# Performance work log

Hardware: AMD Instinct MI355X
Metric: run time of the kernel (lower is better)

## Reference

```python
import jax, jax.numpy as jnp
import numpy as np

B, C, N = 32, 128, 64
HID = 2 * C
STEEPNESS = 50.0


def _bitonic_layers(n):
    """Index pairs (a, b) for each compare-exchange layer of a bitonic sorting
    network, matching diffsort's bitonic_network construction."""
    num_blocks = int(np.log2(n))
    assert n == 2 ** num_blocks
    layers = []
    for block in range(num_blocks):
        for layer in range(block + 1):
            m = 2 ** (block - layer)
            a_idx, b_idx = [], []
            for i in range(0, n, 2 * m):
                for j in range(m):
                    ix = i + j
                    a, b = ix, ix + m
                    # alternate direction within bitonic blocks
                    if (ix // 2 ** (block + 1)) % 2 == 1:
                        a, b = b, a
                    a_idx.append(a)
                    b_idx.append(b)
            layers.append((np.asarray(a_idx), np.asarray(b_idx)))
    return layers

_LAYERS = _bitonic_layers(N)  # 21 layers for N=64


def _diff_sort(scores):
    """Differentiable bitonic sort (diffsort, distribution='cauchy').
    Returns (soft-sorted scores, soft permutation matrix P) with
    sorted = scores @ P; the module applies P via bmm(P, rows)."""
    b, n = scores.shape
    x = scores
    P = jnp.broadcast_to(jnp.eye(n, dtype=scores.dtype), (b, n, n))
    inv_pi = 1.0 / np.pi
    for a_idx, b_idx in _LAYERS:
        xa, xb = x[:, a_idx], x[:, b_idx]
        alpha = jnp.arctan((xb - xa) * STEEPNESS) * inv_pi + 0.5  # Cauchy CDF
        x = x.at[:, a_idx].set(alpha * xa + (1.0 - alpha) * xb)
        x = x.at[:, b_idx].set((1.0 - alpha) * xa + alpha * xb)
        Pa, Pb = P[:, :, a_idx], P[:, :, b_idx]
        al = alpha[:, None, :]
        P = P.at[:, :, a_idx].set(al * Pa + (1.0 - al) * Pb)
        P = P.at[:, :, b_idx].set((1.0 - al) * Pa + al * Pb)
    return x, P


def setup_inputs() -> dict:
    key = jax.random.key(0)
    ks = jax.random.split(key, 9)
    s = 0.05  # keep score magnitudes reasonable under steepness=50
    return {
        "x": jax.random.normal(ks[0], (B, C, N, N), jnp.float32),
        "w1": jax.random.normal(ks[1], (HID, C), jnp.float32) * s,
        "b1": jax.random.normal(ks[2], (HID,), jnp.float32) * s,
        "w2": jax.random.normal(ks[3], (HID, HID), jnp.float32) * s,
        "b2": jax.random.normal(ks[4], (HID,), jnp.float32) * s,
        "w_row": jax.random.normal(ks[5], (HID, N), jnp.float32) * s,
        "b_row": jax.random.normal(ks[6], (1,), jnp.float32) * s,
        "w_col": jax.random.normal(ks[7], (HID, N), jnp.float32) * s,
        "b_col": jax.random.normal(ks[8], (1,), jnp.float32) * s,
    }


def reference(x, w1, b1, w2, b2, w_row, b_row, w_col, b_col):
    # feat_extractor: two 1x1 convs (pointwise channel GEMMs) + ReLU
    h = jax.nn.relu(jnp.einsum('bchw,oc->bohw', x, w1) + b1[None, :, None, None])
    h = jax.nn.relu(jnp.einsum('bchw,oc->bohw', h, w2) + b2[None, :, None, None])

    # row branch: Conv1d(HID*N,1,1) over flattened (channel, width) per row
    row_scores = jnp.einsum('bchw,cw->bh', h, w_row) + b_row  # (B, N)
    _, p_row = _diff_sort(row_scores)
    x = jnp.einsum('bij,bcjk->bcik', p_row, x)  # bmm(P_row, x) per channel

    # col branch: Conv1d(HID*N,1,1) over flattened (channel, height) per column
    col_scores = jnp.einsum('bchw,ch->bw', h, w_col) + b_col  # (B, N)
    _, p_col = _diff_sort(col_scores)
    # original: bmm(P_col, x^T) then view as (B,C,N,N) with NO transpose back
    x = jnp.einsum('bij,bckj->bcik', p_col, x)
    return x
```

## Files before the change

### kernel.cpp

```cpp
#include <hip/hip_runtime.h>
#include <math.h>

#define B_    32
#define C_    128
#define N_    64
#define HID_  256
#define PIX_  4096
#define STEEP 50.0f
#define INV_PI 0.318309886183790671f
#define LDA   40
#define LDH   272
#define LDX   72

typedef unsigned short u16;
typedef __attribute__((ext_vector_type(8))) short bf16x8;
typedef __attribute__((ext_vector_type(4))) float f32x4;

__device__ __forceinline__ u16 f2bf(float f) {
    unsigned int u = __builtin_bit_cast(unsigned int, f);
    unsigned int r = (u + 0x7FFFu + ((u >> 16) & 1u)) >> 16;
    return (u16)r;
}
__device__ __forceinline__ float bf2f(u16 h) {
    unsigned int u = ((unsigned int)h) << 16;
    return __builtin_bit_cast(float, u);
}

__global__ void k0_init(float* __restrict__ col_s, const float* __restrict__ b_col) {
    int i = blockIdx.x * 256 + threadIdx.x;
    if (i < B_ * N_) col_s[i] = b_col[0];
}

__global__ void k_prep(const float* __restrict__ w1, const float* __restrict__ w2,
                       u16* __restrict__ w1h, u16* __restrict__ w1l,
                       u16* __restrict__ w2h, u16* __restrict__ w2l) {
    int i = blockIdx.x * 256 + threadIdx.x;
    if (i < HID_ * C_) {
        float v = w1[i];
        u16 h = f2bf(v);
        w1h[i] = h;
        w1l[i] = f2bf(v - bf2f(h));
    } else {
        int j = i - HID_ * C_;
        if (j < HID_ * HID_) {
            float v = w2[j];
            u16 h = f2bf(v);
            w2h[j] = h;
            w2l[j] = f2bf(v - bf2f(h));
        }
    }
}

__global__ __launch_bounds__(256) void k12_fused(
    const float* __restrict__ x,
    const u16* __restrict__ w1h, const u16* __restrict__ w1l,
    const float* __restrict__ b1,
    const u16* __restrict__ w2h, const u16* __restrict__ w2l,
    const float* __restrict__ b2, const float* __restrict__ w_row,
    const float* __restrict__ b_row, const float* __restrict__ w_col,
    float* __restrict__ row_s, float* __restrict__ col_s) {
    __shared__ __align__(16) u16 Lh1h[64 * LDH];
    __shared__ __align__(16) u16 Lh1l[64 * LDH];
    __shared__ __align__(16) u16 Bh[64 * LDA];
    __shared__ __align__(16) u16 Bl[64 * LDA];
    __shared__ float col_red[64];
    __shared__ float row_red;

    const int t = threadIdx.x;
    const int l = t & 63, w = t >> 6;
    const int col = l & 15, q = l >> 4;
    const int hrow = blockIdx.x;
    const int b = blockIdx.y;
    const int pbase = hrow * 64;
    const float* xb = x + (size_t)b * C_ * PIX_ + pbase;

    if (t < 64) col_red[t] = 0.f;
    if (t == 0) row_red = 0.f;

    f32x4 acc[4][4];
#pragma unroll
    for (int i = 0; i < 4; i++)
#pragma unroll
        for (int j = 0; j < 4; j++) acc[i][j] = (f32x4){0.f, 0.f, 0.f, 0.f};

    const int pt = t & 15, ct = t >> 4;
    for (int kc = 0; kc < 4; kc++) {
        const int c0 = kc * 32;
        {
            const float* r0 = &xb[(size_t)(c0 + 2 * ct) * PIX_ + pt * 4];
            const float* r1 = &xb[(size_t)(c0 + 2 * ct + 1) * PIX_ + pt * 4];
            float4 v0 = *(const float4*)r0;
            float4 v1 = *(const float4*)r1;
            float a0[4] = {v0.x, v0.y, v0.z, v0.w};
            float a1[4] = {v1.x, v1.y, v1.z, v1.w};
#pragma unroll
            for (int j = 0; j < 4; j++) {
                u16 h0 = f2bf(a0[j]), h1 = f2bf(a1[j]);
                u16 l0 = f2bf(a0[j] - bf2f(h0)), l1 = f2bf(a1[j] - bf2f(h1));
                *(unsigned int*)&Bh[(pt * 4 + j) * LDA + 2 * ct] =
                    (unsigned int)h0 | ((unsigned int)h1 << 16);
                *(unsigned int*)&Bl[(pt * 4 + j) * LDA + 2 * ct] =
                    (unsigned int)l0 | ((unsigned int)l1 << 16);
            }
        }
        __syncthreads();
        bf16x8 ah[4], al_[4], bh[4], bl[4];
#pragma unroll
        for (int mf = 0; mf < 4; mf++) {
            size_t ro = (size_t)(64 * w + 16 * mf + col) * C_ + c0 + q * 8;
            ah[mf] = *(const bf16x8*)&w1h[ro];
            al_[mf] = *(const bf16x8*)&w1l[ro];
        }
#pragma unroll
        for (int nt = 0; nt < 4; nt++) {
            bh[nt] = *(const bf16x8*)&Bh[(nt * 16 + col) * LDA + q * 8];
            bl[nt] = *(const bf16x8*)&Bl[(nt * 16 + col) * LDA + q * 8];
        }
#pragma unroll
        for (int mf = 0; mf < 4; mf++)
#pragma unroll
            for (int nt = 0; nt < 4; nt++) {
                acc[mf][nt] = __builtin_amdgcn_mfma_f32_16x16x32_bf16(ah[mf], bh[nt], acc[mf][nt], 0, 0, 0);
                acc[mf][nt] = __builtin_amdgcn_mfma_f32_16x16x32_bf16(ah[mf], bl[nt], acc[mf][nt], 0, 0, 0);
                acc[mf][nt] = __builtin_amdgcn_mfma_f32_16x16x32_bf16(al_[mf], bh[nt], acc[mf][nt], 0, 0, 0);
            }
        __syncthreads();
    }

#pragma unroll
    for (int mf = 0; mf < 4; mf++) {
        int o = 64 * w + 16 * mf + q * 4;
        float bias[4];
#pragma unroll
        for (int r = 0; r < 4; r++) bias[r] = b1[o + r];
#pragma unroll
        for (int nt = 0; nt < 4; nt++) {
            int p = nt * 16 + col;
            u16 hh[4], ll[4];
#pragma unroll
            for (int r = 0; r < 4; r++) {
                float v = fmaxf(acc[mf][nt][r] + bias[r], 0.f);
                u16 h = f2bf(v);
                hh[r] = h;
                ll[r] = f2bf(v - bf2f(h));
            }
            *(unsigned long long*)&Lh1h[p * LDH + o] =
                (unsigned long long)hh[0] | ((unsigned long long)hh[1] << 16) |
                ((unsigned long long)hh[2] << 32) | ((unsigned long long)hh[3] << 48);
            *(unsigned long long*)&Lh1l[p * LDH + o] =
                (unsigned long long)ll[0] | ((unsigned long long)ll[1] << 16) |
                ((unsigned long long)ll[2] << 32) | ((unsigned long long)ll[3] << 48);
        }
    }
    __syncthreads();

    f32x4 acc2[4][4];
#pragma unroll
    for (int i = 0; i < 4; i++)
#pragma unroll
        for (int j = 0; j < 4; j++) acc2[i][j] = (f32x4){0.f, 0.f, 0.f, 0.f};

    for (int kc = 0; kc < 8; kc++) {
        const int k0 = kc * 32;
        bf16x8 ah[4], al_[4], bh[4], bl[4];
#pragma unroll
        for (int mf = 0; mf < 4; mf++) {
            size_t ro = (size_t)(64 * w + 16 * mf + col) * HID_ + k0 + q * 8;
            ah[mf] = *(const bf16x8*)&w2h[ro];
            al_[mf] = *(const bf16x8*)&w2l[ro];
        }
#pragma unroll
        for (int nt = 0; nt < 4; nt++) {
            bh[nt] = *(const bf16x8*)&Lh1h[(nt * 16 + col) * LDH + k0 + q * 8];
            bl[nt] = *(const bf16x8*)&Lh1l[(nt * 16 + col) * LDH + k0 + q * 8];
        }
#pragma unroll
        for (int mf = 0; mf < 4; mf++)
#pragma unroll
            for (int nt = 0; nt < 4; nt++) {
                acc2[mf][nt] = __builtin_amdgcn_mfma_f32_16x16x32_bf16(ah[mf], bh[nt], acc2[mf][nt], 0, 0, 0);
                acc2[mf][nt] = __builtin_amdgcn_mfma_f32_16x16x32_bf16(ah[mf], bl[nt], acc2[mf][nt], 0, 0, 0);
                acc2[mf][nt] = __builtin_amdgcn_mfma_f32_16x16x32_bf16(al_[mf], bh[nt], acc2[mf][nt], 0, 0, 0);
            }
    }

    float rpart = 0.f;
    float cpart[4] = {0.f, 0.f, 0.f, 0.f};
#pragma unroll
    for (int mf = 0; mf < 4; mf++) {
        int o = 64 * w + 16 * mf + q * 4;
#pragma unroll
        for (int r = 0; r < 4; r++) {
            float bias = b2[o + r];
            float wcv = w_col[(o + r) * N_ + hrow];
#pragma unroll
            for (int nt = 0; nt < 4; nt++) {
                int wc = nt * 16 + col;
                float v = fmaxf(acc2[mf][nt][r] + bias, 0.f);
                rpart += v * w_row[(o + r) * N_ + wc];
                cpart[nt] += v * wcv;
            }
        }
    }
#pragma unroll
    for (int off = 32; off; off >>= 1) rpart += __shfl_xor(rpart, off, 64);
    if (l == 0) atomicAdd(&row_red, rpart);
#pragma unroll
    for (int nt = 0; nt < 4; nt++) {
        float cp = cpart[nt];
        cp += __shfl_xor(cp, 16, 64);
        cp += __shfl_xor(cp, 32, 64);
        if (l < 16) atomicAdd(&col_red[nt * 16 + l], cp);
    }
    __syncthreads();
    if (t < 64) atomicAdd(&col_s[b * N_ + t], col_red[t]);
    if (t == 0) row_s[b * N_ + hrow] = b_row[0] + row_red;
}

__global__ __launch_bounds__(256) void k4_diffsort(const float* __restrict__ row_s,
                                                   const float* __restrict__ col_s,
                                                   u16* __restrict__ prow_h, u16* __restrict__ prow_l,
                                                   u16* __restrict__ pcol_h, u16* __restrict__ pcol_l) {
    __shared__ float Ps[64 * 65];
    __shared__ float xs[64];
    __shared__ float als[32];
    const int t = threadIdx.x;
    const int which = blockIdx.x & 1;
    const int b = blockIdx.x >> 1;
    const float* sc = which ? col_s : row_s;
    u16* Ph = which ? pcol_h : prow_h;
    u16* Pl = which ? pcol_l : prow_l;

    if (t < 64) xs[t] = sc[b * 64 + t];
#pragma unroll
    for (int k = 0; k < 16; k++) {
        int idx = t + k * 256;
        int i = idx >> 6, j = idx & 63;
        Ps[i * 65 + j] = (i == j) ? 1.f : 0.f;
    }
    __syncthreads();

    const int r = t & 63, pg = t >> 6;
    for (int bl = 0; bl < 6; bl++) {
        for (int ly = 0; ly <= bl; ly++) {
            int sh = bl - ly;
            int m = 1 << sh;
            if (t < 32) {
                int i = (t >> sh) << (sh + 1);
                int j = t & (m - 1);
                int ix = i + j;
                int a = ix, bi = ix + m;
                if ((ix >> (bl + 1)) & 1) { int tmp = a; a = bi; bi = tmp; }
                float xa = xs[a], xbv = xs[bi];
                float al = atanf((xbv - xa) * STEEP) * INV_PI + 0.5f;
                als[t] = al;
                xs[a] = al * xa + (1.f - al) * xbv;
                xs[bi] = (1.f - al) * xa + al * xbv;
            }
            __syncthreads();
#pragma unroll
            for (int pi = 0; pi < 8; pi++) {
                int p = pg * 8 + pi;
                int i = (p >> sh) << (sh + 1);
                int j = p & (m - 1);
                int ix = i + j;
                int a = ix, bi = ix + m;
                if ((ix >> (bl + 1)) & 1) { int tmp = a; a = bi; bi = tmp; }
                float al = als[p];
                float Pa = Ps[r * 65 + a], Pb = Ps[r * 65 + bi];
                Ps[r * 65 + a] = al * Pa + (1.f - al) * Pb;
                Ps[r * 65 + bi] = (1.f - al) * Pa + al * Pb;
            }
            __syncthreads();
        }
    }
#pragma unroll
    for (int k = 0; k < 16; k++) {
        int idx = t + k * 256;
        int i = idx >> 6, j = idx & 63;
        float v = Ps[i * 65 + j];
        u16 h = f2bf(v);
        Ph[b * 4096 + idx] = h;
        Pl[b * 4096 + idx] = f2bf(v - bf2f(h));
    }
}

__global__ __launch_bounds__(256) void k5_permute(const float* __restrict__ x,
                                                  const u16* __restrict__ pcol_h,
                                                  const u16* __restrict__ pcol_l,
                                                  const u16* __restrict__ prow_h,
                                                  const u16* __restrict__ prow_l,
                                                  float* __restrict__ out) {
    __shared__ __align__(16) u16 Xh[64 * LDX];
    __shared__ __align__(16) u16 Xl[64 * LDX];
    __shared__ __align__(16) u16 Zh[64 * LDX];
    __shared__ __align__(16) u16 Zl[64 * LDX];
    const int t = threadIdx.x;
    const int l = t & 63, w = t >> 6;
    const int col = l & 15, q = l >> 4;
    const int b = blockIdx.y;
    const int cbase = blockIdx.x * 4;
    const int i0 = w * 16;

    const u16* pch = pcol_h + (size_t)b * 4096;
    const u16* pcl = pcol_l + (size_t)b * 4096;
    const u16* prh = prow_h + (size_t)b * 4096;
    const u16* prl = prow_l + (size_t)b * 4096;

    bf16x8 pcA_h[2], pcA_l[2];
#pragma unroll
    for (int ks = 0; ks < 2; ks++) {
        pcA_h[ks] = *(const bf16x8*)&pch[(i0 + col) * 64 + q * 8 + ks * 32];
        pcA_l[ks] = *(const bf16x8*)&pcl[(i0 + col) * 64 + q * 8 + ks * 32];
    }

    for (int ci = 0; ci < 4; ci++) {
        const int c = cbase + ci;
        const float* xc = x + ((size_t)b * C_ + c) * PIX_;
#pragma unroll
        for (int k = 0; k < 4; k++) {
            int f = t + k * 256;
            int rw = f >> 4, c4 = f & 15;
            float4 v = *(const float4*)&xc[f * 4];
            u16 h0 = f2bf(v.x), h1 = f2bf(v.y), h2 = f2bf(v.z), h3 = f2bf(v.w);
            ushort4 hv = {h0, h1, h2, h3};
            ushort4 lv = {f2bf(v.x - bf2f(h0)), f2bf(v.y - bf2f(h1)),
                          f2bf(v.z - bf2f(h2)), f2bf(v.w - bf2f(h3))};
            *(ushort4*)&Xh[rw * LDX + c4 * 4] = hv;
            *(ushort4*)&Xl[rw * LDX + c4 * 4] = lv;
        }
        __syncthreads();

        f32x4 acc[4];
#pragma unroll
        for (int nt = 0; nt < 4; nt++) acc[nt] = (f32x4){0.f, 0.f, 0.f, 0.f};
#pragma unroll
        for (int ks = 0; ks < 2; ks++) {
            bf16x8 ah = pcA_h[ks], al_ = pcA_l[ks];
#pragma unroll
            for (int nt = 0; nt < 4; nt++) {
                bf16x8 bh = *(const bf16x8*)&Xh[(nt * 16 + col) * LDX + q * 8 + ks * 32];
                bf16x8 bl = *(const bf16x8*)&Xl[(nt * 16 + col) * LDX + q * 8 + ks * 32];
                acc[nt] = __builtin_amdgcn_mfma_f32_16x16x32_bf16(ah, bh, acc[nt], 0, 0, 0);
                acc[nt] = __builtin_amdgcn_mfma_f32_16x16x32_bf16(ah, bl, acc[nt], 0, 0, 0);
                acc[nt] = __builtin_amdgcn_mfma_f32_16x16x32_bf16(al_, bh, acc[nt], 0, 0, 0);
            }
        }
#pragma unroll
        for (int nt = 0; nt < 4; nt++)
#pragma unroll
            for (int r = 0; r < 4; r++) {
                float v = acc[nt][r];
                u16 h = f2bf(v);
                int rw = i0 + q * 4 + r;
                Zh[rw * LDX + nt * 16 + col] = h;
                Zl[rw * LDX + nt * 16 + col] = f2bf(v - bf2f(h));
            }

        f32x4 acc2[4];
#pragma unroll
        for (int nt = 0; nt < 4; nt++) acc2[nt] = (f32x4){0.f, 0.f, 0.f, 0.f};
#pragma unroll
        for (int ks = 0; ks < 2; ks++) {
            bf16x8 ah = *(const bf16x8*)&Zh[(i0 + col) * LDX + q * 8 + ks * 32];
            bf16x8 al_ = *(const bf16x8*)&Zl[(i0 + col) * LDX + q * 8 + ks * 32];
#pragma unroll
            for (int nt = 0; nt < 4; nt++) {
                bf16x8 bh = *(const bf16x8*)&prh[(nt * 16 + col) * 64 + q * 8 + ks * 32];
                bf16x8 bl = *(const bf16x8*)&prl[(nt * 16 + col) * 64 + q * 8 + ks * 32];
                acc2[nt] = __builtin_amdgcn_mfma_f32_16x16x32_bf16(ah, bh, acc2[nt], 0, 0, 0);
                acc2[nt] = __builtin_amdgcn_mfma_f32_16x16x32_bf16(ah, bl, acc2[nt], 0, 0, 0);
                acc2[nt] = __builtin_amdgcn_mfma_f32_16x16x32_bf16(al_, bh, acc2[nt], 0, 0, 0);
            }
        }
        float* oc = out + ((size_t)b * C_ + c) * PIX_;
#pragma unroll
        for (int nt = 0; nt < 4; nt++)
#pragma unroll
            for (int r = 0; r < 4; r++)
                oc[(i0 + q * 4 + r) * 64 + nt * 16 + col] = acc2[nt][r];
        __syncthreads();
    }
}

extern "C" void kernel_launch(void* const* d_in, const int* in_sizes, int n_in,
                              void* d_out, int out_size, void* d_ws, size_t ws_size,
                              hipStream_t stream) {
    const float* x = (const float*)d_in[0];
    const float* w1 = (const float*)d_in[1];
    const float* b1 = (const float*)d_in[2];
    const float* w2 = (const float*)d_in[3];
    const float* b2 = (const float*)d_in[4];
    const float* w_row = (const float*)d_in[5];
    const float* b_row = (const float*)d_in[6];
    const float* w_col = (const float*)d_in[7];
    const float* b_col = (const float*)d_in[8];
    float* out = (float*)d_out;

    char* ws = (char*)d_ws;
    u16* w1h = (u16*)(ws);
    u16* w1l = (u16*)(ws + 65536);
    u16* w2h = (u16*)(ws + 131072);
    u16* w2l = (u16*)(ws + 262144);
    float* row_s = (float*)(ws + 393216);
    float* col_s = (float*)(ws + 401408);
    u16* prow_h = (u16*)(ws + 409600);
    u16* prow_l = (u16*)(ws + 671744);
    u16* pcol_h = (u16*)(ws + 933888);
    u16* pcol_l = (u16*)(ws + 1196032);

    hipLaunchKernelGGL(k0_init, dim3(8), dim3(256), 0, stream, col_s, b_col);
    hipLaunchKernelGGL(k_prep, dim3(384), dim3(256), 0, stream, w1, w2, w1h, w1l, w2h, w2l);
    hipLaunchKernelGGL(k12_fused, dim3(64, 32), dim3(256), 0, stream,
                       x, w1h, w1l, b1, w2h, w2l, b2, w_row, b_row, w_col, row_s, col_s);
    hipLaunchKernelGGL(k4_diffsort, dim3(64), dim3(256), 0, stream,
                       row_s, col_s, prow_h, prow_l, pcol_h, pcol_l);
    hipLaunchKernelGGL(k5_permute, dim3(32, 32), dim3(256), 0, stream,
                       x, pcol_h, pcol_l, prow_h, prow_l, out);
}
```

Before: 292.5 us.

## Stage full x tile in shared memory once, swizzle LDS, prefetch weight fragments

The fused double-GEMM kernel now loads all 128 channels of the x tile into shared memory in a single pass with one barrier, instead of one 32-channel chunk per iteration with two barriers each. The x tile and the h1 activations share the same two LDS buffers, using an XOR-rotated (swizzled) index to avoid bank conflicts. The loops are fully unrolled and register-prefetch the next k-chunk of w1/w2 while the current MFMAs run. This removes barriers and hides global-load latency, at the cost of more registers, which could reduce occupancy.

```diff
diff --git a/kernel.cpp b/kernel.cpp
--- a/kernel.cpp
+++ b/kernel.cpp
@@ -8,7 +8,6 @@
 #define PIX_  4096
 #define STEEP 50.0f
 #define INV_PI 0.318309886183790671f
-#define LDA   40
 #define LDH   272
 #define LDX   72
 
@@ -24,6 +23,12 @@
 __device__ __forceinline__ float bf2f(u16 h) {
     unsigned int u = ((unsigned int)h) << 16;
     return __builtin_bit_cast(float, u);
+}
+__device__ __forceinline__ int h1_idx(int p, int k) {
+    return p * LDH + (((k >> 3) + (p & 7)) & 31) * 8 + (k & 7);
+}
+__device__ __forceinline__ int x_idx(int p, int k) {
+    return p * LDH + 128 + (((k >> 3) + (p & 7)) & 15) * 8 + (k & 7);
 }
 
 __global__ void k0_init(float* __restrict__ col_s, const float* __restrict__ b_col) {
@@ -59,10 +64,8 @@
     const float* __restrict__ b2, const float* __restrict__ w_row,
     const float* __restrict__ b_row, const float* __restrict__ w_col,
     float* __restrict__ row_s, float* __restrict__ col_s) {
-    __shared__ __align__(16) u16 Lh1h[64 * LDH];
-    __shared__ __align__(16) u16 Lh1l[64 * LDH];
-    __shared__ __align__(16) u16 Bh[64 * LDA];
-    __shared__ __align__(16) u16 Bl[64 * LDA];
+    __shared__ __align__(16) u16 Lh[64 * LDH];
+    __shared__ __align__(16) u16 Ll[64 * LDH];
     __shared__ float col_red[64];
     __shared__ float row_red;
 
@@ -71,50 +74,62 @@
     const int col = l & 15, q = l >> 4;
     const int hrow = blockIdx.x;
     const int b = blockIdx.y;
-    const int pbase = hrow * 64;
-    const float* xb = x + (size_t)b * C_ * PIX_ + pbase;
+    const float* xb = x + (size_t)b * C_ * PIX_ + hrow * 64;
 
     if (t < 64) col_red[t] = 0.f;
     if (t == 0) row_red = 0.f;
 
-    f32x4 acc[4][4];
-#pragma unroll
-    for (int i = 0; i < 4; i++)
-#pragma unroll
-        for (int j = 0; j < 4; j++) acc[i][j] = (f32x4){0.f, 0.f, 0.f, 0.f};
-
-    const int pt = t & 15, ct = t >> 4;
-    for (int kc = 0; kc < 4; kc++) {
-        const int c0 = kc * 32;
-        {
-            const float* r0 = &xb[(size_t)(c0 + 2 * ct) * PIX_ + pt * 4];
-            const float* r1 = &xb[(size_t)(c0 + 2 * ct + 1) * PIX_ + pt * 4];
-            float4 v0 = *(const float4*)r0;
-            float4 v1 = *(const float4*)r1;
+    {
+        const int pt = t & 15, ct = t >> 4;
+#pragma unroll
+        for (int cc = 0; cc < 4; cc++) {
+            const int c = cc * 32 + 2 * ct;
+            float4 v0 = *(const float4*)&xb[(size_t)c * PIX_ + pt * 4];
+            float4 v1 = *(const float4*)&xb[(size_t)(c + 1) * PIX_ + pt * 4];
             float a0[4] = {v0.x, v0.y, v0.z, v0.w};
             float a1[4] = {v1.x, v1.y, v1.z, v1.w};
 #pragma unroll
             for (int j = 0; j < 4; j++) {
-                u16 h0 = f2bf(a0[j]), h1 = f2bf(a1[j]);
-                u16 l0 = f2bf(a0[j] - bf2f(h0)), l1 = f2bf(a1[j] - bf2f(h1));
-                *(unsigned int*)&Bh[(pt * 4 + j) * LDA + 2 * ct] =
-                    (unsigned int)h0 | ((unsigned int)h1 << 16);
-                *(unsigned int*)&Bl[(pt * 4 + j) * LDA + 2 * ct] =
-                    (unsigned int)l0 | ((unsigned int)l1 << 16);
-            }
-        }
-        __syncthreads();
-        bf16x8 ah[4], al_[4], bh[4], bl[4];
+                int p = pt * 4 + j;
+                u16 h0 = f2bf(a0[j]), h1v = f2bf(a1[j]);
+                u16 l0 = f2bf(a0[j] - bf2f(h0)), l1 = f2bf(a1[j] - bf2f(h1v));
+                int idx = x_idx(p, c);
+                *(unsigned int*)&Lh[idx] = (unsigned int)h0 | ((unsigned int)h1v << 16);
+                *(unsigned int*)&Ll[idx] = (unsigned int)l0 | ((unsigned int)l1 << 16);
+            }
+        }
+    }
+    __syncthreads();
+
+    f32x4 acc[4][4];
+#pragma unroll
+    for (int i = 0; i < 4; i++)
+#pragma unroll
+        for (int j = 0; j < 4; j++) acc[i][j] = (f32x4){0.f, 0.f, 0.f, 0.f};
+
+    bf16x8 ah[4], al_[4];
+#pragma unroll
+    for (int mf = 0; mf < 4; mf++) {
+        size_t ro = (size_t)(64 * w + 16 * mf + col) * C_ + q * 8;
+        ah[mf] = *(const bf16x8*)&w1h[ro];
+        al_[mf] = *(const bf16x8*)&w1l[ro];
+    }
+#pragma unroll
+    for (int kc = 0; kc < 4; kc++) {
+        bf16x8 bh[4], bl[4];
+#pragma unroll
+        for (int nt = 0; nt < 4; nt++) {
+            int idx = x_idx(nt * 16 + col, kc * 32 + q * 8);
+            bh[nt] = *(const bf16x8*)&Lh[idx];
+            bl[nt] = *(const bf16x8*)&Ll[idx];
+        }
+        bf16x8 ahn[4], aln[4];
+        const int kn = (kc + 1) & 3;
 #pragma unroll
         for (int mf = 0; mf < 4; mf++) {
-            size_t ro = (size_t)(64 * w + 16 * mf + col) * C_ + c0 + q * 8;
-            ah[mf] = *(const bf16x8*)&w1h[ro];
-            al_[mf] = *(const bf16x8*)&w1l[ro];
-        }
-#pragma unroll
-        for (int nt = 0; nt < 4; nt++) {
-            bh[nt] = *(const bf16x8*)&Bh[(nt * 16 + col) * LDA + q * 8];
-            bl[nt] = *(const bf16x8*)&Bl[(nt * 16 + col) * LDA + q * 8];
+            size_t ro = (size_t)(64 * w + 16 * mf + col) * C_ + kn * 32 + q * 8;
+            ahn[mf] = *(const bf16x8*)&w1h[ro];
+            aln[mf] = *(const bf16x8*)&w1l[ro];
         }
 #pragma unroll
         for (int mf = 0; mf < 4; mf++)
@@ -124,8 +139,18 @@
                 acc[mf][nt] = __builtin_amdgcn_mfma_f32_16x16x32_bf16(ah[mf], bl[nt], acc[mf][nt], 0, 0, 0);
                 acc[mf][nt] = __builtin_amdgcn_mfma_f32_16x16x32_bf16(al_[mf], bh[nt], acc[mf][nt], 0, 0, 0);
             }
-        __syncthreads();
-    }
+#pragma unroll
+        for (int mf = 0; mf < 4; mf++) { ah[mf] = ahn[mf]; al_[mf] = aln[mf]; }
+    }
+
+    bf16x8 ah2[4], al2[4];
+#pragma unroll
+    for (int mf = 0; mf < 4; mf++) {
+        size_t ro = (size_t)(64 * w + 16 * mf + col) * HID_ + q * 8;
+        ah2[mf] = *(const bf16x8*)&w2h[ro];
+        al2[mf] = *(const bf16x8*)&w2l[ro];
+    }
+    __syncthreads();
 
 #pragma unroll
     for (int mf = 0; mf < 4; mf++) {
@@ -144,10 +169,11 @@
                 hh[r] = h;
                 ll[r] = f2bf(v - bf2f(h));
             }
-            *(unsigned long long*)&Lh1h[p * LDH + o] =
+            int idx = h1_idx(p, o);
+            *(unsigned long long*)&Lh[idx] =
                 (unsigned long long)hh[0] | ((unsigned long long)hh[1] << 16) |
                 ((unsigned long long)hh[2] << 32) | ((unsigned long long)hh[3] << 48);
-            *(unsigned long long*)&Lh1l[p * LDH + o] =
+            *(unsigned long long*)&Ll[idx] =
                 (unsigned long long)ll[0] | ((unsigned long long)ll[1] << 16) |
                 ((unsigned long long)ll[2] << 32) | ((unsigned long long)ll[3] << 48);
         }
@@ -160,28 +186,33 @@
 #pragma unroll
         for (int j = 0; j < 4; j++) acc2[i][j] = (f32x4){0.f, 0.f, 0.f, 0.f};
 
+#pragma unroll
     for (int kc = 0; kc < 8; kc++) {
-        const int k0 = kc * 32;
-        bf16x8 ah[4], al_[4], bh[4], bl[4];
+        bf16x8 bh[4], bl[4];
+#pragma unroll
+        for (int nt = 0; nt < 4; nt++) {
+            int idx = h1_idx(nt * 16 + col, kc * 32 + q * 8);
+            bh[nt] = *(const bf16x8*)&Lh[idx];
+            bl[nt] = *(const bf16x8*)&Ll[idx];
+        }
+        bf16x8 ahn[4], aln[4];
+        const int kn = (kc + 1) & 7;
 #pragma unroll
         for (int mf = 0; mf < 4; mf++) {
-            size_t ro = (size_t)(64 * w + 16 * mf + col) * HID_ + k0 + q * 8;
-            ah[mf] = *(const bf16x8*)&w2h[ro];
-            al_[mf] = *(const bf16x8*)&w2l[ro];
-        }
-#pragma unroll
-        for (int nt = 0; nt < 4; nt++) {
-            bh[nt] = *(const bf16x8*)&Lh1h[(nt * 16 + col) * LDH + k0 + q * 8];
-            bl[nt] = *(const bf16x8*)&Lh1l[(nt * 16 + col) * LDH + k0 + q * 8];
+            size_t ro = (size_t)(64 * w + 16 * mf + col) * HID_ + kn * 32 + q * 8;
+            ahn[mf] = *(const bf16x8*)&w2h[ro];
+            aln[mf] = *(const bf16x8*)&w2l[ro];
         }
 #pragma unroll
         for (int mf = 0; mf < 4; mf++)
 #pragma unroll
             for (int nt = 0; nt < 4; nt++) {
-                acc2[mf][nt] = __builtin_amdgcn_mfma_f32_16x16x32_bf16(ah[mf], bh[nt], acc2[mf][nt], 0, 0, 0);
-                acc2[mf][nt] = __builtin_amdgcn_mfma_f32_16x16x32_bf16(ah[mf], bl[nt], acc2[mf][nt], 0, 0, 0);
-                acc2[mf][nt] = __builtin_amdgcn_mfma_f32_16x16x32_bf16(al_[mf], bh[nt], acc2[mf][nt], 0, 0, 0);
-            }
+                acc2[mf][nt] = __builtin_amdgcn_mfma_f32_16x16x32_bf16(ah2[mf], bh[nt], acc2[mf][nt], 0, 0, 0);
+                acc2[mf][nt] = __builtin_amdgcn_mfma_f32_16x16x32_bf16(ah2[mf], bl[nt], acc2[mf][nt], 0, 0, 0);
+                acc2[mf][nt] = __builtin_amdgcn_mfma_f32_16x16x32_bf16(al2[mf], bh[nt], acc2[mf][nt], 0, 0, 0);
+            }
+#pragma unroll
+        for (int mf = 0; mf < 4; mf++) { ah2[mf] = ahn[mf]; al2[mf] = aln[mf]; }
     }
 
     float rpart = 0.f;
```

After: 291.5 us. About the same (-0.3%).
